# Kernel tuning notes

Measured on AMD Instinct MI355X. Metric: run time of the kernel, lower is better.

The kernel has to match this reference:

```python
import jax, jax.numpy as jnp
import numpy as np

B = 256      # number of graphs
IN = 128     # input_dim
FD = 256     # feature_dim (dims[1])
HID = 256    # hidden_dim of attention block (dims[2])
OUT = 128    # final output dim (dims[3])
TXT = 512    # text_emb_dim

LENGTHS = np.asarray(128 + (np.arange(B) % 256), dtype=np.int64)  # ragged lens 128..383
N = int(LENGTHS.sum())  # 65408 total nodes
LMAX = int(LENGTHS.max())  # 383


def setup_inputs() -> dict:
    key = jax.random.key(0)
    ks = jax.random.split(key, 16)
    s = 0.02
    return {
        "input": jax.random.normal(ks[0], (N, IN), jnp.float32),
        "text_emb": jax.random.normal(ks[1], (B, TXT), jnp.float32),
        "repeat_list": jnp.asarray(LENGTHS),
        # layer 0: Linear(IN -> FD)
        "W0": jax.random.normal(ks[2], (IN, FD), jnp.float32) * s,
        "b0": jax.random.normal(ks[3], (FD,), jnp.float32) * s,
        # cross-attention block params
        "Wq": jax.random.normal(ks[4], (TXT, FD), jnp.float32) * s,
        "bq": jax.random.normal(ks[5], (FD,), jnp.float32) * s,
        "Wk": jax.random.normal(ks[6], (FD, FD), jnp.float32) * s,
        "bk": jax.random.normal(ks[7], (FD,), jnp.float32) * s,
        "Wv": jax.random.normal(ks[8], (FD, FD), jnp.float32) * s,
        "bv": jax.random.normal(ks[9], (FD,), jnp.float32) * s,
        "Wo": jax.random.normal(ks[10], (FD, HID), jnp.float32) * s,
        "bo": jax.random.normal(ks[11], (HID,), jnp.float32) * s,
        # layer 2: Linear(HID -> OUT), last layer (no activation)
        "W2": jax.random.normal(ks[12], (HID, OUT), jnp.float32) * s,
        "b2": jax.random.normal(ks[13], (OUT,), jnp.float32) * s,
    }


def _cross_attention(h, text_emb, repeat_list, Wq, bq, Wk, bk, Wv, bv, Wo, bo):
    # h: [N, FD] packed ragged node features; repeat_list: [B] lengths (constant ints)
    n = h.shape[0]
    b = repeat_list.shape[0]
    fd = h.shape[1]
    # pad ragged -> [B, LMAX, FD] (pad value 0) + validity mask
    seg = jnp.repeat(jnp.arange(b), repeat_list, total_repeat_length=n)  # [N] graph id
    offsets = jnp.cumsum(repeat_list) - repeat_list                      # [B] start of each graph
    pos = jnp.arange(n) - offsets[seg]                                   # [N] within-graph pos
    padded = jnp.zeros((b, LMAX, fd), h.dtype).at[seg, pos].set(h)
    valid = jnp.arange(LMAX)[None, :] < repeat_list[:, None]             # [B, L]

    q = text_emb @ Wq + bq                              # [B, FD]
    k = (padded @ Wk + bk) * valid[..., None]           # masked_fill(mask==0, 0)
    v = (padded @ Wv + bv) * valid[..., None]

    # query is broadcast identically over the padded-length axis, so each row of the
    # [L, L] score matrix is the same vector: scores[b, j] = q[b] . k[b, j]
    scores = jnp.einsum('bf,bjf->bj', q, k)             # [B, L]
    scores = jnp.where(valid, scores, -jnp.inf)         # mask invalid columns j
    p = jax.nn.softmax(scores, axis=-1)                 # [B, L]
    # output = attention^T @ value with identical rows => out[b,j,:] = p[b,j] * sum_i v[b,i,:]
    v_sum = v.sum(axis=1)                               # [B, FD] (padded rows already zero)
    out_pad = p[..., None] * v_sum[:, None, :]          # [B, L, FD]
    out_nodes = out_pad[seg, pos]                       # unpad-concat -> [N, FD]
    return out_nodes @ Wo + bo                          # [N, HID]


def reference(input, text_emb, repeat_list, W0, b0, Wq, bq, Wk, bk, Wv, bv, Wo, bo, W2, b2):
    h = jax.nn.relu(input @ W0 + b0)                                     # layer 0 + relu
    h = _cross_attention(h, text_emb, repeat_list, Wq, bq, Wk, bk, Wv, bv, Wo, bo)
    h = jax.nn.relu(h)                                                   # layer 1 + relu
    return h @ W2 + b2                                                   # layer 2 (last, no act)
```

## Files before the change

kernel.cpp:

```cpp
#include <hip/hip_runtime.h>
#include <math.h>

#define B_G   256
#define IN_D  128
#define FD    256
#define HID   256
#define OUT_D 128
#define TXT   512
#define XKS   136

typedef short bf16x8 __attribute__((ext_vector_type(8)));
typedef float f32x4  __attribute__((ext_vector_type(4)));

__device__ __forceinline__ unsigned bf_rne(float x) {
    unsigned u = __float_as_uint(x);
    u += 0x7fffu + ((u >> 16) & 1u);
    return u >> 16;
}
__device__ __forceinline__ float bf_to_f(unsigned h) {
    return __uint_as_float(h << 16);
}
__device__ __forceinline__ void split2(float a0, float a1, unsigned& hp, unsigned& lp) {
    unsigned h0 = bf_rne(a0), h1 = bf_rne(a1);
    float r0 = a0 - bf_to_f(h0), r1 = a1 - bf_to_f(h1);
    hp = h0 | (h1 << 16);
    lp = bf_rne(r0) | (bf_rne(r1) << 16);
}

__global__ __launch_bounds__(256) void k_prepA(
    const float* __restrict__ text_emb, const float* __restrict__ Wq,
    const float* __restrict__ bq, const float* __restrict__ Wk,
    const float* __restrict__ W0, const int* __restrict__ lens,
    float* __restrict__ qk, int* __restrict__ offsets, float* __restrict__ hsum,
    unsigned short* __restrict__ W0sH, unsigned short* __restrict__ W0sL)
{
    int blk = blockIdx.x, t = threadIdx.x;
    __shared__ float te[TXT];
    __shared__ float q[FD];
    __shared__ int   sc[B_G];

    if (blk < 256) {
        int b = blk;
        hsum[b * FD + t] = 0.f;
        for (int i = t; i < TXT; i += 256) te[i] = text_emb[(size_t)b * TXT + i];
        __syncthreads();
        float acc = bq[t];
        for (int k = 0; k < TXT; k++) acc = fmaf(te[k], Wq[k * FD + t], acc);
        q[t] = acc;
        __syncthreads();
        float a2 = 0.f;
        for (int f = 0; f < FD; f++) a2 = fmaf(Wk[t * FD + f], q[f], a2);
        qk[b * FD + t] = a2;
    } else if (blk < 260) {
        int e = (blk - 256) * 256 + t;
        int kc = e >> 8, c = e & 255;
        size_t base = (size_t)(kc * 256 + c) * 32;
        for (int kk = 0; kk < 32; kk++) {
            float v = W0[(size_t)(kc * 32 + kk) * FD + c];
            unsigned h = bf_rne(v);
            float r = v - bf_to_f(h);
            W0sH[base + kk] = (unsigned short)h;
            W0sL[base + kk] = (unsigned short)bf_rne(r);
        }
    } else {
        sc[t] = lens[t];
        __syncthreads();
        for (int d = 1; d < 256; d <<= 1) {
            int v = (t >= d) ? sc[t - d] : 0;
            __syncthreads();
            sc[t] += v;
            __syncthreads();
        }
        offsets[t + 1] = sc[t];
        if (t == 0) offsets[0] = 0;
    }
}

__global__ __launch_bounds__(256, 4) void k_l0_mfma(
    const float* __restrict__ X,
    const unsigned short* __restrict__ W0sH, const unsigned short* __restrict__ W0sL,
    const float* __restrict__ b0, const float* __restrict__ qk,
    const int* __restrict__ offsets,
    float* __restrict__ scores, float* __restrict__ hsum)
{
    int b = blockIdx.y;
    int off = offsets[b], len = offsets[b + 1] - off;
    int n0 = blockIdx.x * 64;
    if (n0 >= len) return;
    int nvalid = min(64, len - n0);

    __shared__ __align__(16) unsigned short XsH[64 * XKS], XsL[64 * XKS];
    __shared__ float qks[FD];
    __shared__ float bsh[FD];
    __shared__ float red[4][64];

    int tid = threadIdx.x;
    int lane = tid & 63, w = tid >> 6;
    int ln = lane & 15, quad = lane >> 4;

    qks[tid] = qk[b * FD + tid];
    bsh[tid] = b0[tid];

    {
        int node_s = tid >> 2, ks = (tid & 3) * 32;
        const float4* Xr4 = (const float4*)(X + (size_t)(off + n0 + node_s) * IN_D + ks);
        bool v = (node_s < nvalid);
#pragma unroll
        for (int g = 0; g < 4; g++) {
            float4 a, c4;
            if (v) { a = Xr4[2 * g]; c4 = Xr4[2 * g + 1]; }
            else   { a = make_float4(0.f, 0.f, 0.f, 0.f); c4 = a; }
            uint4 hq, lq;
            split2(a.x,  a.y,  hq.x, lq.x);
            split2(a.z,  a.w,  hq.y, lq.y);
            split2(c4.x, c4.y, hq.z, lq.z);
            split2(c4.z, c4.w, hq.w, lq.w);
            *(uint4*)&XsH[node_s * XKS + ks + g * 8] = hq;
            *(uint4*)&XsL[node_s * XKS + ks + g * 8] = lq;
        }
    }
    __syncthreads();

    f32x4 acc[4][4] = {};
#pragma unroll
    for (int kc = 0; kc < 4; kc++) {
        bf16x8 AH[4], AL[4];
#pragma unroll
        for (int i = 0; i < 4; i++) {
            AH[i] = *(const bf16x8*)&XsH[(16 * i + ln) * XKS + kc * 32 + quad * 8];
            AL[i] = *(const bf16x8*)&XsL[(16 * i + ln) * XKS + kc * 32 + quad * 8];
        }
#pragma unroll
        for (int j = 0; j < 4; j++) {
            int c = 64 * w + 16 * j + ln;
            size_t base = (size_t)(kc * 256 + c) * 32 + quad * 8;
            bf16x8 BH = *(const bf16x8*)&W0sH[base];
            bf16x8 BL = *(const bf16x8*)&W0sL[base];
#pragma unroll
            for (int i = 0; i < 4; i++) {
                acc[i][j] = __builtin_amdgcn_mfma_f32_16x16x32_bf16(AH[i], BH, acc[i][j], 0, 0, 0);
                acc[i][j] = __builtin_amdgcn_mfma_f32_16x16x32_bf16(AH[i], BL, acc[i][j], 0, 0, 0);
                acc[i][j] = __builtin_amdgcn_mfma_f32_16x16x32_bf16(AL[i], BH, acc[i][j], 0, 0, 0);
            }
        }
    }

    float sp[4][4];
    float cs[4] = {0.f, 0.f, 0.f, 0.f};
#pragma unroll
    for (int i = 0; i < 4; i++)
#pragma unroll
        for (int r = 0; r < 4; r++) sp[i][r] = 0.f;

#pragma unroll
    for (int i = 0; i < 4; i++)
#pragma unroll
        for (int j = 0; j < 4; j++) {
            int c = 64 * w + 16 * j + ln;
            float bb = bsh[c], qv = qks[c];
#pragma unroll
            for (int r = 0; r < 4; r++) {
                int node = 16 * i + 4 * quad + r;
                float h = acc[i][j][r] + bb;
                h = (h > 0.f && node < nvalid) ? h : 0.f;
                sp[i][r] = fmaf(h, qv, sp[i][r]);
                cs[j] += h;
            }
        }
#pragma unroll
    for (int i = 0; i < 4; i++)
#pragma unroll
        for (int r = 0; r < 4; r++) {
            float s = sp[i][r];
            s += __shfl_xor(s, 1); s += __shfl_xor(s, 2);
            s += __shfl_xor(s, 4); s += __shfl_xor(s, 8);
            sp[i][r] = s;
        }
    if (ln == 0) {
#pragma unroll
        for (int i = 0; i < 4; i++)
#pragma unroll
            for (int r = 0; r < 4; r++)
                red[w][16 * i + 4 * quad + r] = sp[i][r];
    }
#pragma unroll
    for (int j = 0; j < 4; j++) {
        float s = cs[j];
        s += __shfl_xor(s, 16); s += __shfl_xor(s, 32);
        if (quad == 0) atomicAdd(&hsum[b * FD + 64 * w + 16 * j + ln], s);
    }
    __syncthreads();
    if (tid < 64 && tid < nvalid)
        scores[off + n0 + tid] = red[0][tid] + red[1][tid] + red[2][tid] + red[3][tid];
}

__global__ __launch_bounds__(1024) void k_graph_walk(
    const float* __restrict__ scores, const float* __restrict__ hsum,
    const float* __restrict__ Wv, const float* __restrict__ bv,
    const float* __restrict__ Wo, const float* __restrict__ bo,
    const float* __restrict__ W2, const float* __restrict__ b2,
    const int* __restrict__ offsets, float* __restrict__ Y)
{
    int b = blockIdx.x, tid = threadIdx.x;
    int off = offsets[b], len = offsets[b + 1] - off;
    int t = tid & 255, g = tid >> 8;
    int lane = tid & 63;

    __shared__ float redm[16], reds[16];
    __shared__ float hs[FD], vs[FD];
    __shared__ float part[4][FD];
    __shared__ float wv2[HID], boS[HID], b2s[OUT_D];
    __shared__ __align__(16) float tOrig[256];
    __shared__ float tS[256], dwS[256], dbS[256];
    __shared__ int   kS[256];
    __shared__ int   cnt[257], startS[257];
    __shared__ float A0s[OUT_D], C0s[OUT_D];
    __shared__ float segA[8][OUT_D], segC[8][OUT_D];
    __shared__ __align__(16) int4 ops4[704];

    if (g == 0) { boS[t] = bo[t]; hs[t] = hsum[b * FD + t]; }
    if (tid < OUT_D) b2s[tid] = b2[tid];
    if (tid <= 256) cnt[tid] = 0;
    float s_n = (tid < len) ? scores[off + tid] : -INFINITY;

    float m = s_n;
#pragma unroll
    for (int d = 1; d < 64; d <<= 1) m = fmaxf(m, __shfl_xor(m, d));
    if ((tid & 63) == 0) redm[tid >> 6] = m;
    __syncthreads();
    m = -INFINITY;
#pragma unroll
    for (int k = 0; k < 16; k++) m = fmaxf(m, redm[k]);

    float e_n = (tid < len) ? expf(s_n - m) : 0.f;
    float s = e_n;
#pragma unroll
    for (int d = 1; d < 64; d <<= 1) s += __shfl_xor(s, d);
    if ((tid & 63) == 0) reds[tid >> 6] = s;
    __syncthreads();
    s = 0.f;
#pragma unroll
    for (int k = 0; k < 16; k++) s += reds[k];
    float dinv = 1.0f / s;

    float acc = (g == 0) ? (float)len * bv[t] : 0.f;
    for (int f = 64 * g; f < 64 * g + 64; f++) acc = fmaf(hs[f], Wv[f * FD + t], acc);
    part[g][t] = acc;
    __syncthreads();
    if (g == 0) vs[t] = part[0][t] + part[1][t] + part[2][t] + part[3][t];
    __syncthreads();
    float a2 = 0.f;
    for (int f = 64 * g; f < 64 * g + 64; f++) a2 = fmaf(vs[f], Wo[f * HID + t], a2);
    part[g][t] = a2;
    __syncthreads();
    if (g == 0) wv2[t] = part[0][t] + part[1][t] + part[2][t] + part[3][t];
    __syncthreads();

    bool real = false;
    if (tid < 256) {
        float wv = wv2[tid], bvv = boS[tid];
        bool isev = (wv > 0.f && bvv < 0.f) || (wv < 0.f && bvv > 0.f);
        float tk = isev ? (-bvv / wv) : INFINITY;
        real = isev && (tk < INFINITY);
        tOrig[tid] = real ? tk : INFINITY;
    }
    __syncthreads();

    if (tid < 256) {
        float tk = tOrig[tid];
        int r = 0;
        const float4* t4 = (const float4*)tOrig;
        for (int j4 = 0; j4 < 64; ++j4) {
            float4 tj = t4[j4];
            int e0 = 4 * j4;
            r += (tj.x < tk || (tj.x == tk && (e0 + 0) < tid)) ? 1 : 0;
            r += (tj.y < tk || (tj.y == tk && (e0 + 1) < tid)) ? 1 : 0;
            r += (tj.z < tk || (tj.z == tk && (e0 + 2) < tid)) ? 1 : 0;
            r += (tj.w < tk || (tj.w == tk && (e0 + 3) < tid)) ? 1 : 0;
        }
        tS[r] = tk;
        kS[r] = tid;
        float wv = wv2[tid], bvv = boS[tid];
        dwS[r] = real ? fabsf(wv) : 0.f;
        dbS[r] = real ? -fabsf(bvv) : 0.f;
    }
    {
        int q = tid >> 7, c = tid & 127;
        float pa = 0.f, pc = 0.f;
        for (int k = q * 32; k < q * 32 + 32; ++k) {
            float v = W2[(size_t)k * OUT_D + c];
            float wv = wv2[k], bvv = boS[k];
            bool ini = (bvv > 0.f) || (bvv == 0.f && wv > 0.f);
            pa = fmaf(ini ? wv : 0.f, v, pa);
            pc = fmaf(ini ? bvv : 0.f, v, pc);
        }
        segA[q][c] = pa; segC[q][c] = pc;
    }
    int nE = __syncthreads_count(real);

    float p_n = 0.f; int r_n = 0;
    if (tid < len) {
        p_n = e_n * dinv;
        int r = 0;
#pragma unroll
        for (int st = 128; st > 0; st >>= 1)
            if (tS[r + st - 1] < p_n) r += st;
        r_n = r;
        atomicAdd(&cnt[r], 1);
    }
    if (tid < OUT_D) {
        float sa = 0.f, sc2 = 0.f;
#pragma unroll
        for (int q = 0; q < 8; q++) { sa += segA[q][tid]; sc2 += segC[q][tid]; }
        A0s[tid] = sa; C0s[tid] = sc2;
    }
    __syncthreads();

    if (tid < 64) {
        int l = tid;
        int v0 = cnt[4 * l], v1 = cnt[4 * l + 1], v2 = cnt[4 * l + 2], v3 = cnt[4 * l + 3];
        int s0 = v0, s1 = s0 + v1, s2 = s1 + v2, s3 = s2 + v3;
        int run = s3;
#pragma unroll
        for (int d = 1; d < 64; d <<= 1) {
            int t2 = __shfl_up(run, d);
            if (l >= d) run += t2;
        }
        int base = run - s3;
        startS[4 * l + 0] = base;      cnt[4 * l + 0] = base;
        startS[4 * l + 1] = base + s0; cnt[4 * l + 1] = base + s0;
        startS[4 * l + 2] = base + s1; cnt[4 * l + 2] = base + s1;
        startS[4 * l + 3] = base + s2; cnt[4 * l + 3] = base + s2;
        if (l == 63) { startS[256] = base + s3; cnt[256] = base + s3; }
    }
    __syncthreads();

    int L    = len + nE;
    int Lpad = (L + 7) & ~7;
    int Lseg = ((Lpad + 63) >> 6) << 3;
    int sg = tid >> 7, c = tid & 127;

    if (tid < len) {
        int slot = atomicAdd(&cnt[r_n], 1);
        int pos = slot + r_n;
        ops4[pos] = make_int4(__float_as_int(p_n), 0, tid, 0);
    }
    if (tid < nE) {
        int pos = startS[tid + 1] + tid;
        ops4[pos] = make_int4(__float_as_int(dwS[tid]), __float_as_int(dbS[tid]), -1, kS[tid]);
    }
    for (int i = L + tid; i < 704; i += 1024)
        ops4[i] = make_int4(0, 0, -1, 0);
    __syncthreads();

    int i0 = sg * Lseg;
    int4 cur = ops4[i0 + lane];
    int4 nxt = ops4[i0 + 64 + lane];

    {
        float dA = 0.f, dC = 0.f;
        for (int ii = 0; ii < Lseg; ii += 8) {
            int4 rc = (ii < 64) ? cur : nxt;
            int bb = ii & 63;
#pragma unroll
            for (int d = 0; d < 8; ++d) {
                int nI = __builtin_amdgcn_readlane(rc.z, bb + d);
                if (nI < 0) {
                    float aI = __uint_as_float((unsigned)__builtin_amdgcn_readlane(rc.x, bb + d));
                    float bI = __uint_as_float((unsigned)__builtin_amdgcn_readlane(rc.y, bb + d));
                    int   kI = __builtin_amdgcn_readlane(rc.w, bb + d);
                    float v = W2[(size_t)kI * OUT_D + c];
                    dA = fmaf(aI, v, dA);
                    dC = fmaf(bI, v, dC);
                }
            }
        }
        segA[sg][c] = dA; segC[sg][c] = dC;
    }
    __syncthreads();

    {
        float A = A0s[c], C = C0s[c];
        for (int s2 = 0; s2 < sg; ++s2) { A += segA[s2][c]; C += segC[s2][c]; }
        float b2v = b2s[c];
        float* Yb = Y + (size_t)off * OUT_D + c;

        float rV[8];
#pragma unroll
        for (int d = 0; d < 8; ++d) {
            int nU = __builtin_amdgcn_readlane(cur.z, d);
            int kU = __builtin_amdgcn_readlane(cur.w, d);
            if (nU < 0) rV[d] = W2[(size_t)kU * OUT_D + c];
            else        rV[d] = 0.f;
        }
        for (int ii = 0; ii < Lseg; ii += 8) {
            int4 rc = (ii < 64) ? cur : nxt;
            int bc = ii & 63;
            int4 rp = (ii + 8 < 64) ? cur : nxt;
            int bp = (ii + 8) & 63;
#pragma unroll
            for (int d = 0; d < 8; ++d) {
                float aI = __uint_as_float((unsigned)__builtin_amdgcn_readlane(rc.x, bc + d));
                int   nI = __builtin_amdgcn_readlane(rc.z, bc + d);
                int   np = __builtin_amdgcn_readlane(rp.z, bp + d);
                int   kp = __builtin_amdgcn_readlane(rp.w, bp + d);
                float vv = rV[d];
                if (nI >= 0) {
                    Yb[(size_t)nI * OUT_D] = fmaf(aI, A, C) + b2v;
                } else {
                    float bI = __uint_as_float((unsigned)__builtin_amdgcn_readlane(rc.y, bc + d));
                    A = fmaf(aI, vv, A);
                    C = fmaf(bI, vv, C);
                }
                if (np < 0) rV[d] = W2[(size_t)kp * OUT_D + c];
            }
        }
    }
}

extern "C" void kernel_launch(void* const* d_in, const int* in_sizes, int n_in,
                              void* d_out, int out_size, void* d_ws, size_t ws_size,
                              hipStream_t stream)
{
    const float* X        = (const float*)d_in[0];
    const float* text_emb = (const float*)d_in[1];
    const int*   lens     = (const int*)d_in[2];
    const float* W0       = (const float*)d_in[3];
    const float* b0       = (const float*)d_in[4];
    const float* Wq       = (const float*)d_in[5];
    const float* bq       = (const float*)d_in[6];
    const float* Wk       = (const float*)d_in[7];
    const float* Wv       = (const float*)d_in[9];
    const float* bv       = (const float*)d_in[10];
    const float* Wo       = (const float*)d_in[11];
    const float* bo       = (const float*)d_in[12];
    const float* W2       = (const float*)d_in[13];
    const float* b2       = (const float*)d_in[14];
    float* Y = (float*)d_out;

    char* base = (char*)d_ws;
    size_t o = 0;
    int*   offsets = (int*)(base + o);            o += 1088;
    float* qkbuf   = (float*)(base + o);          o += 262144;
    float* hsum    = (float*)(base + o);          o += 262144;
    float* scores  = (float*)(base + o);          o += 262144;
    unsigned short* W0sH = (unsigned short*)(base + o); o += 65536;
    unsigned short* W0sL = (unsigned short*)(base + o); o += 65536;

    k_prepA<<<261, 256, 0, stream>>>(text_emb, Wq, bq, Wk, W0, lens,
                                     qkbuf, offsets, hsum, W0sH, W0sL);
    k_l0_mfma<<<dim3(6, B_G), 256, 0, stream>>>(X, W0sH, W0sL, b0, qkbuf, offsets, scores, hsum);
    k_graph_walk<<<B_G, 1024, 0, stream>>>(scores, hsum, Wv, bv, Wo, bo, W2, b2, offsets, Y);
}
```

Before: 205.0 us.

## Split graph walk into stats kernel and two-block-per-graph walk kernel

The fused per-graph kernel is split in two. k_stats does the softmax and the Wv/Wo vector products and writes probabilities and per-graph vectors to workspace. k_walk launches two 512-thread blocks per graph; each block redoes the full segment prefix (event sort, dA/dC sweep with prefetched W2 rows) and then writes only its half of the output segments. Node ranking now uses a deterministic O(n) comparison sort in place of atomic slot assignment. The intent is more blocks and better occupancy in the bandwidth-bound output phase, at the cost of an extra launch, a workspace round-trip and duplicated prefix work.

```diff
diff --git a/kernel.cpp b/kernel.cpp
--- a/kernel.cpp
+++ b/kernel.cpp
@@ -194,21 +194,67 @@
         scores[off + n0 + tid] = red[0][tid] + red[1][tid] + red[2][tid] + red[3][tid];
 }
 
-__global__ __launch_bounds__(1024) void k_graph_walk(
+__global__ __launch_bounds__(1024) void k_stats(
     const float* __restrict__ scores, const float* __restrict__ hsum,
     const float* __restrict__ Wv, const float* __restrict__ bv,
-    const float* __restrict__ Wo, const float* __restrict__ bo,
-    const float* __restrict__ W2, const float* __restrict__ b2,
-    const int* __restrict__ offsets, float* __restrict__ Y)
+    const float* __restrict__ Wo, const int* __restrict__ offsets,
+    float* __restrict__ pbuf, float* __restrict__ wvecb)
 {
     int b = blockIdx.x, tid = threadIdx.x;
+    int t = tid & 255, g = tid >> 8;
     int off = offsets[b], len = offsets[b + 1] - off;
-    int t = tid & 255, g = tid >> 8;
-    int lane = tid & 63;
-
     __shared__ float redm[16], reds[16];
     __shared__ float hs[FD], vs[FD];
     __shared__ float part[4][FD];
+
+    if (g == 0) hs[t] = hsum[b * FD + t];
+    float s_n = (tid < len) ? scores[off + tid] : -INFINITY;
+
+    float m = s_n;
+#pragma unroll
+    for (int d = 1; d < 64; d <<= 1) m = fmaxf(m, __shfl_xor(m, d));
+    if ((tid & 63) == 0) redm[tid >> 6] = m;
+    __syncthreads();
+    m = -INFINITY;
+#pragma unroll
+    for (int k = 0; k < 16; k++) m = fmaxf(m, redm[k]);
+
+    float e_n = (tid < len) ? expf(s_n - m) : 0.f;
+    float s = e_n;
+#pragma unroll
+    for (int d = 1; d < 64; d <<= 1) s += __shfl_xor(s, d);
+    if ((tid & 63) == 0) reds[tid >> 6] = s;
+    __syncthreads();
+    s = 0.f;
+#pragma unroll
+    for (int k = 0; k < 16; k++) s += reds[k];
+    float dinv = 1.0f / s;
+    if (tid < len) pbuf[off + tid] = e_n * dinv;
+
+    float acc = (g == 0) ? (float)len * bv[t] : 0.f;
+    for (int f = 64 * g; f < 64 * g + 64; f++) acc = fmaf(hs[f], Wv[f * FD + t], acc);
+    part[g][t] = acc;
+    __syncthreads();
+    if (g == 0) vs[t] = part[0][t] + part[1][t] + part[2][t] + part[3][t];
+    __syncthreads();
+    float a2 = 0.f;
+    for (int f = 64 * g; f < 64 * g + 64; f++) a2 = fmaf(vs[f], Wo[f * HID + t], a2);
+    part[g][t] = a2;
+    __syncthreads();
+    if (g == 0) wvecb[b * HID + t] = part[0][t] + part[1][t] + part[2][t] + part[3][t];
+}
+
+__global__ __launch_bounds__(512) void k_walk(
+    const float* __restrict__ pbuf, const float* __restrict__ wvecb,
+    const float* __restrict__ bo, const float* __restrict__ W2,
+    const float* __restrict__ b2, const int* __restrict__ offsets,
+    float* __restrict__ Y)
+{
+    int bx = blockIdx.x;
+    int b = bx >> 1, half = bx & 1;
+    int tid = threadIdx.x, lane = tid & 63;
+    int off = offsets[b], len = offsets[b + 1] - off;
+
     __shared__ float wv2[HID], boS[HID], b2s[OUT_D];
     __shared__ __align__(16) float tOrig[256];
     __shared__ float tS[256], dwS[256], dbS[256];
@@ -216,44 +262,13 @@
     __shared__ int   cnt[257], startS[257];
     __shared__ float A0s[OUT_D], C0s[OUT_D];
     __shared__ float segA[8][OUT_D], segC[8][OUT_D];
+    __shared__ __align__(16) float ps_l[512];
     __shared__ __align__(16) int4 ops4[704];
 
-    if (g == 0) { boS[t] = bo[t]; hs[t] = hsum[b * FD + t]; }
+    if (tid < 256) { wv2[tid] = wvecb[b * HID + tid]; boS[tid] = bo[tid]; }
     if (tid < OUT_D) b2s[tid] = b2[tid];
     if (tid <= 256) cnt[tid] = 0;
-    float s_n = (tid < len) ? scores[off + tid] : -INFINITY;
-
-    float m = s_n;
-#pragma unroll
-    for (int d = 1; d < 64; d <<= 1) m = fmaxf(m, __shfl_xor(m, d));
-    if ((tid & 63) == 0) redm[tid >> 6] = m;
-    __syncthreads();
-    m = -INFINITY;
-#pragma unroll
-    for (int k = 0; k < 16; k++) m = fmaxf(m, redm[k]);
-
-    float e_n = (tid < len) ? expf(s_n - m) : 0.f;
-    float s = e_n;
-#pragma unroll
-    for (int d = 1; d < 64; d <<= 1) s += __shfl_xor(s, d);
-    if ((tid & 63) == 0) reds[tid >> 6] = s;
-    __syncthreads();
-    s = 0.f;
-#pragma unroll
-    for (int k = 0; k < 16; k++) s += reds[k];
-    float dinv = 1.0f / s;
-
-    float acc = (g == 0) ? (float)len * bv[t] : 0.f;
-    for (int f = 64 * g; f < 64 * g + 64; f++) acc = fmaf(hs[f], Wv[f * FD + t], acc);
-    part[g][t] = acc;
-    __syncthreads();
-    if (g == 0) vs[t] = part[0][t] + part[1][t] + part[2][t] + part[3][t];
-    __syncthreads();
-    float a2 = 0.f;
-    for (int f = 64 * g; f < 64 * g + 64; f++) a2 = fmaf(vs[f], Wo[f * HID + t], a2);
-    part[g][t] = a2;
-    __syncthreads();
-    if (g == 0) wv2[t] = part[0][t] + part[1][t] + part[2][t] + part[3][t];
+    ps_l[tid] = (tid < len) ? pbuf[off + tid] : INFINITY;
     __syncthreads();
 
     bool real = false;
@@ -287,7 +302,7 @@
     {
         int q = tid >> 7, c = tid & 127;
         float pa = 0.f, pc = 0.f;
-        for (int k = q * 32; k < q * 32 + 32; ++k) {
+        for (int k = q * 64; k < q * 64 + 64; ++k) {
             float v = W2[(size_t)k * OUT_D + c];
             float wv = wv2[k], bvv = boS[k];
             bool ini = (bvv > 0.f) || (bvv == 0.f && wv > 0.f);
@@ -298,9 +313,9 @@
     }
     int nE = __syncthreads_count(real);
 
-    float p_n = 0.f; int r_n = 0;
+    float p_n = ps_l[tid];
+    int r_n = 0;
     if (tid < len) {
-        p_n = e_n * dinv;
         int r = 0;
 #pragma unroll
         for (int st = 128; st > 0; st >>= 1)
@@ -309,10 +324,8 @@
         atomicAdd(&cnt[r], 1);
     }
     if (tid < OUT_D) {
-        float sa = 0.f, sc2 = 0.f;
-#pragma unroll
-        for (int q = 0; q < 8; q++) { sa += segA[q][tid]; sc2 += segC[q][tid]; }
-        A0s[tid] = sa; C0s[tid] = sc2;
+        A0s[tid] = segA[0][tid] + segA[1][tid] + segA[2][tid] + segA[3][tid];
+        C0s[tid] = segC[0][tid] + segC[1][tid] + segC[2][tid] + segC[3][tid];
     }
     __syncthreads();
 
@@ -327,82 +340,103 @@
             if (l >= d) run += t2;
         }
         int base = run - s3;
-        startS[4 * l + 0] = base;      cnt[4 * l + 0] = base;
-        startS[4 * l + 1] = base + s0; cnt[4 * l + 1] = base + s0;
-        startS[4 * l + 2] = base + s1; cnt[4 * l + 2] = base + s1;
-        startS[4 * l + 3] = base + s2; cnt[4 * l + 3] = base + s2;
-        if (l == 63) { startS[256] = base + s3; cnt[256] = base + s3; }
+        startS[4 * l + 0] = base;
+        startS[4 * l + 1] = base + s0;
+        startS[4 * l + 2] = base + s1;
+        startS[4 * l + 3] = base + s2;
+        if (l == 63) startS[256] = base + s3;
     }
     __syncthreads();
 
     int L    = len + nE;
     int Lpad = (L + 7) & ~7;
     int Lseg = ((Lpad + 63) >> 6) << 3;
-    int sg = tid >> 7, c = tid & 127;
 
     if (tid < len) {
-        int slot = atomicAdd(&cnt[r_n], 1);
-        int pos = slot + r_n;
+        int rk = 0;
+        const float4* p4 = (const float4*)ps_l;
+        for (int j4 = 0; j4 < 128; ++j4) {
+            float4 pj = p4[j4];
+            int e0 = 4 * j4;
+            rk += (pj.x < p_n || (pj.x == p_n && (e0 + 0) < tid)) ? 1 : 0;
+            rk += (pj.y < p_n || (pj.y == p_n && (e0 + 1) < tid)) ? 1 : 0;
+            rk += (pj.z < p_n || (pj.z == p_n && (e0 + 2) < tid)) ? 1 : 0;
+            rk += (pj.w < p_n || (pj.w == p_n && (e0 + 3) < tid)) ? 1 : 0;
+        }
+        int pos = r_n + rk;
         ops4[pos] = make_int4(__float_as_int(p_n), 0, tid, 0);
     }
     if (tid < nE) {
         int pos = startS[tid + 1] + tid;
         ops4[pos] = make_int4(__float_as_int(dwS[tid]), __float_as_int(dbS[tid]), -1, kS[tid]);
     }
-    for (int i = L + tid; i < 704; i += 1024)
+    for (int i = L + tid; i < 704; i += 512)
         ops4[i] = make_int4(0, 0, -1, 0);
     __syncthreads();
 
-    int i0 = sg * Lseg;
-    int4 cur = ops4[i0 + lane];
-    int4 nxt = ops4[i0 + 64 + lane];
-
     {
-        float dA = 0.f, dC = 0.f;
+        int sgd = tid >> 6;
+        int i0 = sgd * Lseg;
+        int4 cur = ops4[i0 + lane];
+        int4 nxt = ops4[i0 + 64 + lane];
+        const float* W2a = W2 + lane;
+        const float* W2b = W2 + 64 + lane;
+        float dA0 = 0.f, dC0 = 0.f, dA1 = 0.f, dC1 = 0.f;
+        float rV0[8], rV1[8];
+#pragma unroll
+        for (int d = 0; d < 8; ++d) {
+            int kU = __builtin_amdgcn_readlane(cur.w, d);
+            rV0[d] = W2a[(size_t)kU * OUT_D];
+            rV1[d] = W2b[(size_t)kU * OUT_D];
+        }
         for (int ii = 0; ii < Lseg; ii += 8) {
-            int4 rc = (ii < 64) ? cur : nxt;
-            int bb = ii & 63;
+            int4 rc = (ii < 64) ? cur : nxt;      int bc = ii & 63;
+            int4 rp = (ii + 8 < 64) ? cur : nxt;  int bp = (ii + 8) & 63;
 #pragma unroll
             for (int d = 0; d < 8; ++d) {
-                int nI = __builtin_amdgcn_readlane(rc.z, bb + d);
+                int   nI = __builtin_amdgcn_readlane(rc.z, bc + d);
+                float aI = __uint_as_float((unsigned)__builtin_amdgcn_readlane(rc.x, bc + d));
+                float bI = __uint_as_float((unsigned)__builtin_amdgcn_readlane(rc.y, bc + d));
+                int   kp = __builtin_amdgcn_readlane(rp.w, bp + d);
+                float v0 = rV0[d], v1 = rV1[d];
                 if (nI < 0) {
-                    float aI = __uint_as_float((unsigned)__builtin_amdgcn_readlane(rc.x, bb + d));
-                    float bI = __uint_as_float((unsigned)__builtin_amdgcn_readlane(rc.y, bb + d));
-                    int   kI = __builtin_amdgcn_readlane(rc.w, bb + d);
-                    float v = W2[(size_t)kI * OUT_D + c];
-                    dA = fmaf(aI, v, dA);
-                    dC = fmaf(bI, v, dC);
+                    dA0 = fmaf(aI, v0, dA0); dC0 = fmaf(bI, v0, dC0);
+                    dA1 = fmaf(aI, v1, dA1); dC1 = fmaf(bI, v1, dC1);
                 }
+                rV0[d] = W2a[(size_t)kp * OUT_D];
+                rV1[d] = W2b[(size_t)kp * OUT_D];
             }
         }
-        segA[sg][c] = dA; segC[sg][c] = dC;
+        segA[sgd][lane] = dA0;      segC[sgd][lane] = dC0;
+        segA[sgd][lane + 64] = dA1; segC[sgd][lane + 64] = dC1;
     }
     __syncthreads();
 
     {
+        int sg = 4 * half + (tid >> 7);
+        int c = tid & 127;
         float A = A0s[c], C = C0s[c];
         for (int s2 = 0; s2 < sg; ++s2) { A += segA[s2][c]; C += segC[s2][c]; }
         float b2v = b2s[c];
         float* Yb = Y + (size_t)off * OUT_D + c;
+        int i0 = sg * Lseg;
+        int4 cur = ops4[i0 + lane];
+        int4 nxt = ops4[i0 + 64 + lane];
+        const float* W2c = W2 + c;
 
         float rV[8];
 #pragma unroll
         for (int d = 0; d < 8; ++d) {
-            int nU = __builtin_amdgcn_readlane(cur.z, d);
             int kU = __builtin_amdgcn_readlane(cur.w, d);
-            if (nU < 0) rV[d] = W2[(size_t)kU * OUT_D + c];
-            else        rV[d] = 0.f;
+            rV[d] = W2c[(size_t)kU * OUT_D];
         }
         for (int ii = 0; ii < Lseg; ii += 8) {
-            int4 rc = (ii < 64) ? cur : nxt;
-            int bc = ii & 63;
-            int4 rp = (ii + 8 < 64) ? cur : nxt;
-            int bp = (ii + 8) & 63;
+            int4 rc = (ii < 64) ? cur : nxt;      int bc = ii & 63;
+            int4 rp = (ii + 8 < 64) ? cur : nxt;  int bp = (ii + 8) & 63;
 #pragma unroll
             for (int d = 0; d < 8; ++d) {
                 float aI = __uint_as_float((unsigned)__builtin_amdgcn_readlane(rc.x, bc + d));
                 int   nI = __builtin_amdgcn_readlane(rc.z, bc + d);
-                int   np = __builtin_amdgcn_readlane(rp.z, bp + d);
                 int   kp = __builtin_amdgcn_readlane(rp.w, bp + d);
                 float vv = rV[d];
                 if (nI >= 0) {
@@ -412,7 +446,7 @@
                     A = fmaf(aI, vv, A);
                     C = fmaf(bI, vv, C);
                 }
-                if (np < 0) rV[d] = W2[(size_t)kp * OUT_D + c];
+                rV[d] = W2c[(size_t)kp * OUT_D];
             }
         }
     }
@@ -444,11 +478,14 @@
     float* qkbuf   = (float*)(base + o);          o += 262144;
     float* hsum    = (float*)(base + o);          o += 262144;
     float* scores  = (float*)(base + o);          o += 262144;
+    float* pbuf    = (float*)(base + o);          o += 262144;
+    float* wvecb   = (float*)(base + o);          o += 262144;
     unsigned short* W0sH = (unsigned short*)(base + o); o += 65536;
     unsigned short* W0sL = (unsigned short*)(base + o); o += 65536;
 
     k_prepA<<<261, 256, 0, stream>>>(text_emb, Wq, bq, Wk, W0, lens,
                                      qkbuf, offsets, hsum, W0sH, W0sL);
     k_l0_mfma<<<dim3(6, B_G), 256, 0, stream>>>(X, W0sH, W0sL, b0, qkbuf, offsets, scores, hsum);
-    k_graph_walk<<<B_G, 1024, 0, stream>>>(scores, hsum, Wv, bv, Wo, bo, W2, b2, offsets, Y);
-}
+    k_stats<<<B_G, 1024, 0, stream>>>(scores, hsum, Wv, bv, Wo, offsets, pbuf, wvecb);
+    k_walk<<<512, 512, 0, stream>>>(pbuf, wvecb, bo, W2, b2, offsets, Y);
+}
```

After: 216.9 us. 1.06x slower.
